# Optimization experiments

Measured on AMD Instinct MI355X. Metric: run time of the kernel, lower is better.

## Reference

```python
import jax, jax.numpy as jnp
import numpy as np

B, L, D, H = 4, 1024, 1024, 16
DH = D // H
NEG = -1e9


def setup_inputs() -> dict:
    key = jax.random.key(0)
    ks = jax.random.split(key, 8)
    sequence = jax.random.normal(ks[0], (B, L, D), dtype=jnp.float32)
    # additive padding mask: all tokens valid -> zeros
    padding_mask = jnp.zeros((B, 1, 1, L), dtype=jnp.float32)
    # additive causal dependency mask: -1e9 above the diagonal
    causal = jnp.triu(jnp.full((L, L), NEG, dtype=jnp.float32), k=1)
    dependency_mask = causal[None, None, :, :]
    scale = 1.0 / np.sqrt(D)
    Wq = jax.random.normal(ks[1], (D, D), dtype=jnp.float32) * scale
    Wk = jax.random.normal(ks[2], (D, D), dtype=jnp.float32) * scale
    Wv = jax.random.normal(ks[3], (D, D), dtype=jnp.float32) * scale
    bq = jnp.zeros((D,), dtype=jnp.float32)
    bk = jnp.zeros((D,), dtype=jnp.float32)
    bv = jnp.zeros((D,), dtype=jnp.float32)
    return {"sequence": sequence, "padding_mask": padding_mask,
            "dependency_mask": dependency_mask,
            "Wq": Wq, "bq": bq, "Wk": Wk, "bk": bk, "Wv": Wv, "bv": bv}


def reference(sequence, padding_mask, dependency_mask, Wq, bq, Wk, bk, Wv, bv):
    b, l, d = sequence.shape
    h, dh = H, d // H
    # Q/K/V linear projections (torch Linear: x @ W^T + b)
    q = (sequence @ Wq.T + bq).reshape(b, l, h, dh)
    k = (sequence @ Wk.T + bk).reshape(b, l, h, dh)
    v = (sequence @ Wv.T + bv).reshape(b, l, h, dh)
    # scaled dot-product scores: [B, H, L, L]
    scores = jnp.einsum('blhd,bmhd->bhlm', q, k) / jnp.sqrt(jnp.float32(dh))
    scores = scores + padding_mask + dependency_mask
    attn = jax.nn.softmax(scores, axis=-1)
    # dropout is identity in eval mode (training=False)
    out = jnp.einsum('bhlm,bmhd->blhd', attn, v)
    return out.reshape(b, l, d)
```

## Files before the change

kernel.cpp:

```cpp
#include <hip/hip_runtime.h>
#include <hip/hip_bf16.h>


#define LL 1024

typedef __attribute__((ext_vector_type(8))) short short8;
typedef __attribute__((ext_vector_type(4))) float floatx4;

__device__ __forceinline__ float bf2f(unsigned short u) {
    return __uint_as_float(((unsigned int)u) << 16);
}
__device__ __forceinline__ unsigned short f2bf(float f) {
    unsigned int x = __float_as_uint(f);
    unsigned int r = x + 0x7fffu + ((x >> 16) & 1u);
    return (unsigned short)(r >> 16);
}

#if __has_builtin(__builtin_amdgcn_global_load_lds)
#define HAVE_GLL 1
typedef __attribute__((address_space(1))) unsigned int as1_u32;
typedef __attribute__((address_space(3))) unsigned int as3_u32;
__device__ __forceinline__ void gll16(const void* g, void* l) {
    __builtin_amdgcn_global_load_lds((const as1_u32*)g, (as3_u32*)l, 16, 0, 0);
}
#endif

#if __has_builtin(__builtin_amdgcn_exp2f)
#define EXP2F(x) __builtin_amdgcn_exp2f(x)
#else
#define EXP2F(x) exp2f(x)
#endif

__global__ __launch_bounds__(256) void conv_in(
    const float* __restrict__ seq, const float* __restrict__ wq,
    const float* __restrict__ wk,  const float* __restrict__ wv,
    const float* __restrict__ bq,  const float* __restrict__ bk,
    const float* __restrict__ bv,  const float* __restrict__ pm,
    unsigned short* __restrict__ ws)
{
    unsigned int t = blockIdx.x * 256u + threadIdx.x;
    if (t >= 918400u) return;
    unsigned int e = t * 8u;
    const float* src; unsigned int idx; unsigned short* dst; float scale = 1.0f;
    if (e < 4194304u)      { src = seq; idx = e;            dst = ws + 12582912u; }
    else if (e < 5242880u) { src = wq;  idx = e - 4194304u; dst = ws + 16777216u; }
    else if (e < 6291456u) { src = wk;  idx = e - 5242880u; dst = ws + 17825792u; }
    else if (e < 7340032u) { src = wv;  idx = e - 6291456u; dst = ws + 18874368u; }
    else if (e < 7341056u) { src = bq;  idx = e - 7340032u; dst = ws + 20971520u; }
    else if (e < 7342080u) { src = bk;  idx = e - 7341056u; dst = ws + 20972544u; }
    else if (e < 7343104u) { src = bv;  idx = e - 7342080u; dst = ws + 20973568u; }
    else { src = pm; idx = e - 7343104u; dst = ws + 20974592u; scale = 1.4426950f; }
    float4 a = *(const float4*)(src + idx);
    float4 c = *(const float4*)(src + idx + 4);
    uint4 st;
    st.x = (unsigned)f2bf(a.x * scale) | ((unsigned)f2bf(a.y * scale) << 16);
    st.y = (unsigned)f2bf(a.z * scale) | ((unsigned)f2bf(a.w * scale) << 16);
    st.z = (unsigned)f2bf(c.x * scale) | ((unsigned)f2bf(c.y * scale) << 16);
    st.w = (unsigned)f2bf(c.z * scale) | ((unsigned)f2bf(c.w * scale) << 16);
    *(uint4*)(dst + idx) = st;
}

__global__ __launch_bounds__(512, 2) void qkv_proj(
    const unsigned short* __restrict__ X,
    const unsigned short* __restrict__ Wcat,
    const unsigned short* __restrict__ bcat,
    unsigned short* __restrict__ dst_base)
{
    __shared__ __align__(16) unsigned short SMEM[3 * 16384 + 2 * 12288];
    unsigned short (*Abuf)[16384] = (unsigned short (*)[16384])SMEM;
    unsigned short (*Bbuf)[12288] = (unsigned short (*)[12288])(SMEM + 3 * 16384);

    const int tid  = threadIdx.x;
    const int lane = tid & 63;
    const int wave = tid >> 6;
    const int quad = lane >> 4, r16 = lane & 15;
    const int wr = wave >> 1, wc = wave & 1;
    const int m0 = blockIdx.x * 256;
    const int n0 = blockIdx.y * 192;

    const int r3   = lane >> 3;
    const int stc  = ((lane & 7) ^ r3) << 3;
    const int seg0a = wave * 4;
    const int seg0b = wave * 3;

    const unsigned short* Asrc = X    + (size_t)(m0 + seg0a * 8 + r3) * 1024 + stc;
    const unsigned short* Bsrc = Wcat + (size_t)(n0 + seg0b * 8 + r3) * 1024 + stc;

    floatx4 acc[4][6];
#pragma unroll
    for (int i = 0; i < 4; ++i)
#pragma unroll
        for (int j = 0; j < 6; ++j)
#pragma unroll
            for (int r = 0; r < 4; ++r) acc[i][j][r] = 0.f;

#ifdef HAVE_GLL
#pragma unroll
    for (int c = 0; c < 4; ++c) gll16(Asrc + (size_t)c * 8192, &Abuf[0][(seg0a + c) * 512]);
#pragma unroll
    for (int c = 0; c < 3; ++c) gll16(Bsrc + (size_t)c * 8192, &Bbuf[0][(seg0b + c) * 512]);
#pragma unroll
    for (int c = 0; c < 4; ++c) gll16(Asrc + (size_t)c * 8192 + 64, &Abuf[1][(seg0a + c) * 512]);
    asm volatile("s_waitcnt vmcnt(4)" ::: "memory");
    __builtin_amdgcn_s_barrier();
#endif

    int sA = 0;
    for (int t = 0; t < 16; ++t) {
        const unsigned short* Ac = &Abuf[sA][0];
        const unsigned short* Bc = &Bbuf[t & 1][0];
        const int aoff = (wr * 64 + r16) * 64;
        const int boff = (wc * 96 + r16) * 64;
        const int c0 = ((0 + quad) ^ (r16 & 7)) << 3;
        const int c1 = ((4 + quad) ^ (r16 & 7)) << 3;
        const int sAw = (sA == 0) ? 2 : (sA - 1);
        const size_t koA = (size_t)((t + 2) << 6);
        short8 a[2], b[6];

#ifndef HAVE_GLL
        __syncthreads();
#pragma unroll
        for (int c = 0; c < 4; ++c)
            *(uint4*)&Abuf[0][(seg0a + c) * 512 + lane * 8] =
                *(const uint4*)(Asrc + (size_t)c * 8192 + (t << 6));
#pragma unroll
        for (int c = 0; c < 3; ++c)
            *(uint4*)&Bbuf[0][(seg0b + c) * 512 + lane * 8] =
                *(const uint4*)(Bsrc + (size_t)c * 8192 + (t << 6));
        __syncthreads();
        Ac = &Abuf[0][0]; Bc = &Bbuf[0][0];
#endif

#pragma unroll
        for (int j = 0; j < 6; ++j) b[j] = *(const short8*)&Bc[boff + j * 1024 + c0];
#pragma unroll
        for (int i = 0; i < 2; ++i) a[i] = *(const short8*)&Ac[aoff + i * 1024 + c0];
#ifdef HAVE_GLL
        if (t < 15) {
            const int sBw = (t + 1) & 1;
            const size_t ko = (size_t)((t + 1) << 6);
#pragma unroll
            for (int c = 0; c < 3; ++c)
                gll16(Bsrc + (size_t)c * 8192 + ko, &Bbuf[sBw][(seg0b + c) * 512]);
        }
        __builtin_amdgcn_s_barrier();
        asm volatile("s_waitcnt lgkmcnt(0)" ::: "memory");
#endif
        __builtin_amdgcn_s_setprio(1);
#pragma unroll
        for (int i = 0; i < 2; ++i)
#pragma unroll
            for (int j = 0; j < 6; ++j)
                acc[i][j] = __builtin_amdgcn_mfma_f32_16x16x32_bf16(a[i], b[j], acc[i][j], 0, 0, 0);
        __builtin_amdgcn_s_setprio(0);
#ifdef HAVE_GLL
        __builtin_amdgcn_s_barrier();
#endif

#pragma unroll
        for (int i = 0; i < 2; ++i) a[i] = *(const short8*)&Ac[aoff + (2 + i) * 1024 + c0];
#ifdef HAVE_GLL
        if (t < 14) {
#pragma unroll
            for (int c = 0; c < 2; ++c)
                gll16(Asrc + (size_t)c * 8192 + koA, &Abuf[sAw][(seg0a + c) * 512]);
        }
        __builtin_amdgcn_s_barrier();
        asm volatile("s_waitcnt lgkmcnt(0)" ::: "memory");
#endif
        __builtin_amdgcn_s_setprio(1);
#pragma unroll
        for (int i = 0; i < 2; ++i)
#pragma unroll
            for (int j = 0; j < 6; ++j)
                acc[2 + i][j] = __builtin_amdgcn_mfma_f32_16x16x32_bf16(a[i], b[j], acc[2 + i][j], 0, 0, 0);
        __builtin_amdgcn_s_setprio(0);
#ifdef HAVE_GLL
        __builtin_amdgcn_s_barrier();
#endif

#pragma unroll
        for (int j = 0; j < 6; ++j) b[j] = *(const short8*)&Bc[boff + j * 1024 + c1];
#pragma unroll
        for (int i = 0; i < 2; ++i) a[i] = *(const short8*)&Ac[aoff + i * 1024 + c1];
#ifdef HAVE_GLL
        if (t < 14) {
#pragma unroll
            for (int c = 2; c < 4; ++c)
                gll16(Asrc + (size_t)c * 8192 + koA, &Abuf[sAw][(seg0a + c) * 512]);
        }
        __builtin_amdgcn_s_barrier();
        asm volatile("s_waitcnt lgkmcnt(0)" ::: "memory");
#endif
        __builtin_amdgcn_s_setprio(1);
#pragma unroll
        for (int i = 0; i < 2; ++i)
#pragma unroll
            for (int j = 0; j < 6; ++j)
                acc[i][j] = __builtin_amdgcn_mfma_f32_16x16x32_bf16(a[i], b[j], acc[i][j], 0, 0, 0);
        __builtin_amdgcn_s_setprio(0);
#ifdef HAVE_GLL
        __builtin_amdgcn_s_barrier();
#endif

#pragma unroll
        for (int i = 0; i < 2; ++i) a[i] = *(const short8*)&Ac[aoff + (2 + i) * 1024 + c1];
#ifdef HAVE_GLL
        __builtin_amdgcn_s_barrier();
        asm volatile("s_waitcnt lgkmcnt(0)" ::: "memory");
#endif
        __builtin_amdgcn_s_setprio(1);
#pragma unroll
        for (int i = 0; i < 2; ++i)
#pragma unroll
            for (int j = 0; j < 6; ++j)
                acc[2 + i][j] = __builtin_amdgcn_mfma_f32_16x16x32_bf16(a[i], b[j], acc[2 + i][j], 0, 0, 0);
        __builtin_amdgcn_s_setprio(0);
#ifdef HAVE_GLL
        if (t < 14) {
            asm volatile("s_waitcnt vmcnt(4)" ::: "memory");
        } else if (t == 14) {
            asm volatile("s_waitcnt vmcnt(0)" ::: "memory");
        }
        __builtin_amdgcn_s_barrier();
#endif
        sA = (sA == 2) ? 0 : (sA + 1);
    }

    unsigned short* Cs = SMEM;
    const int b_ = m0 >> 10, l0_ = m0 & 1023;
#pragma unroll
    for (int j = 0; j < 6; ++j) {
        int n = n0 + wc * 96 + j * 16 + r16;
        int z = n >> 10;
        int nn = n & 1023;
        float bvf = bf2f(bcat[n]);
        int h = nn >> 6, d = nn & 63;
        if (z == 2) {
            unsigned short* dst = dst_base + (size_t)2 * (4096u * 1024u);
#pragma unroll
            for (int i = 0; i < 4; ++i) {
                int m_base = m0 + wr * 64 + i * 16 + quad * 4;
                int bb = m_base >> 10, l0 = m_base & 1023;
                ushort4 st;
                st.x = f2bf(acc[i][j][0] + bvf); st.y = f2bf(acc[i][j][1] + bvf);
                st.z = f2bf(acc[i][j][2] + bvf); st.w = f2bf(acc[i][j][3] + bvf);
                *(ushort4*)&dst[(((size_t)(bb * 16 + h)) * 64 + d) * 1024 + l0] = st;
            }
        } else {
            float sc = (z == 0) ? 0.18033688f : 1.0f;
            int col = wc * 96 + j * 16 + r16;
#pragma unroll
            for (int i = 0; i < 4; ++i) {
                int mrow = wr * 64 + i * 16 + quad * 4;
#pragma unroll
                for (int r = 0; r < 4; ++r)
                    Cs[(mrow + r) * 208 + col] = f2bf((acc[i][j][r] + bvf) * sc);
            }
        }
    }
    asm volatile("s_waitcnt lgkmcnt(0)" ::: "memory");
    __builtin_amdgcn_s_barrier();
#pragma unroll
    for (int g = 0; g < 3; ++g) {
        int ng = n0 + g * 64;
        int zg = ng >> 10;
        if (zg < 2) {
            int hg = (ng & 1023) >> 6;
            unsigned short* dq = dst_base + (size_t)zg * (4096u * 1024u)
                               + (((size_t)(b_ * 16 + hg)) * 1024 + l0_) * 64;
#pragma unroll
            for (int it = 0; it < 4; ++it) {
                int row = it * 64 + (tid >> 3);
                uint4 v = *(const uint4*)&Cs[row * 208 + g * 64 + (tid & 7) * 8];
                *(uint4*)(dq + (size_t)row * 64 + (tid & 7) * 8) = v;
            }
        }
    }
}

__global__ __launch_bounds__(256) void attn(
    const unsigned short* __restrict__ Qw,
    const unsigned short* __restrict__ Kw,
    const unsigned short* __restrict__ Vt_g,
    const unsigned short* __restrict__ pmask,
    float* __restrict__ out)
{
    __shared__ __align__(16) unsigned short KsF[8192];
    __shared__ __align__(16) unsigned short VsF[8192];
    __shared__ __align__(16) unsigned short PsF[4][2048];

    const int tid  = threadIdx.x;
    const int lane = tid & 63;
    const int wave = tid >> 6;
    const int quad = lane >> 4, r16 = lane & 15;

    const int bid  = blockIdx.x;
    const int half = bid >> 8, idx = bid & 255;
    const int bh   = idx & 63;
    const int qb   = idx >> 6;
    const int qi   = half ? (7 - qb) : qb;
    const int b    = bh >> 4, h = bh & 15;
    const int q0   = qi << 7;

    const size_t base = (size_t)bh * (1024 * 64);
    const unsigned short* Qg = Qw + base;
    const unsigned short* Kg = Kw + base;
    const unsigned short* Vg = Vt_g + base;

    const int kst_r3  = lane >> 3;
    const int kst_col = ((lane & 7) ^ kst_r3) << 3;
    const int vst_r   = lane >> 4;

    short8 aq[2][2];
#pragma unroll
    for (int f = 0; f < 2; ++f) {
        int qrow = q0 + f * 64 + wave * 16 + r16;
        aq[f][0] = *(const short8*)(Qg + (size_t)qrow * 64 + quad * 8);
        aq[f][1] = *(const short8*)(Qg + (size_t)qrow * 64 + 32 + quad * 8);
    }

    short8 ones;
#pragma unroll
    for (int i = 0; i < 8; ++i) ones[i] = (short)0x3f80;

    floatx4 ol[2];
    floatx4 o[2][4];
#pragma unroll
    for (int f = 0; f < 2; ++f)
#pragma unroll
        for (int r = 0; r < 4; ++r) ol[f][r] = 0.f;
#pragma unroll
    for (int f = 0; f < 2; ++f)
#pragma unroll
        for (int j = 0; j < 4; ++j)
#pragma unroll
            for (int r = 0; r < 4; ++r) o[f][j][r] = 0.f;

    for (int kt = 0; kt <= qi; ++kt) {
        float pm2[8];
#pragma unroll
        for (int j = 0; j < 8; ++j)
            pm2[j] = bf2f(pmask[b * LL + kt * 128 + j * 16 + r16]) - 12.0f;

        __syncthreads();
#ifdef HAVE_GLL
#pragma unroll
        for (int c2 = 0; c2 < 4; ++c2) {
            int seg = wave * 4 + c2;
            int krow = seg * 8 + kst_r3;
            gll16(Kg + (size_t)(kt * 128 + krow) * 64 + kst_col, &KsF[seg * 512]);
            int vrow = seg * 4 + vst_r;
            int vcol = (((lane & 15) ^ (vrow & 7))) << 3;
            gll16(Vg + (size_t)vrow * 1024 + kt * 128 + vcol, &VsF[seg * 512]);
        }
#else
#pragma unroll
        for (int c2 = 0; c2 < 4; ++c2) {
            int seg = wave * 4 + c2;
            int krow = seg * 8 + kst_r3;
            *(uint4*)&KsF[seg * 512 + lane * 8] =
                *(const uint4*)(Kg + (size_t)(kt * 128 + krow) * 64 + kst_col);
            int vrow = seg * 4 + vst_r;
            int vcol = (((lane & 15) ^ (vrow & 7))) << 3;
            *(uint4*)&VsF[seg * 512 + lane * 8] =
                *(const uint4*)(Vg + (size_t)vrow * 1024 + kt * 128 + vcol);
        }
#endif
        __syncthreads();

#pragma unroll
        for (int f = 0; f < 2; ++f) {
            floatx4 s[8];
#pragma unroll
            for (int j = 0; j < 8; ++j) {
                float pv = pm2[j];
#pragma unroll
                for (int r = 0; r < 4; ++r) s[j][r] = pv;
            }
#pragma unroll
            for (int j = 0; j < 8; ++j) {
                short8 bk0 = *(const short8*)&KsF[(j * 16 + r16) * 64 + (((0 * 4 + quad) ^ (r16 & 7)) << 3)];
                s[j] = __builtin_amdgcn_mfma_f32_16x16x32_bf16(aq[f][0], bk0, s[j], 0, 0, 0);
                short8 bk1 = *(const short8*)&KsF[(j * 16 + r16) * 64 + (((1 * 4 + quad) ^ (r16 & 7)) << 3)];
                s[j] = __builtin_amdgcn_mfma_f32_16x16x32_bf16(aq[f][1], bk1, s[j], 0, 0, 0);
            }

            if (kt == qi) {
                const int my_q = q0 + f * 64 + wave * 16 + quad * 4;
#pragma unroll
                for (int j = 0; j < 8; ++j) {
                    int key = kt * 128 + j * 16 + r16;
#pragma unroll
                    for (int r = 0; r < 4; ++r)
                        if (key > my_q + r) s[j][r] -= 1.0e9f;
                }
            }

#pragma unroll
            for (int j = 0; j < 8; ++j) {
                int key = j * 16 + r16;
                int ab = ((key >> 5) << 9) + (((key >> 3) & 3) << 7) + (key & 7) + (quad << 5);
#pragma unroll
                for (int r = 0; r < 4; ++r) {
                    float p = EXP2F(s[j][r]);
                    PsF[wave][ab + (r << 3)] = (unsigned short)(__float_as_uint(p) >> 16);
                }
            }
            asm volatile("s_waitcnt lgkmcnt(0)" ::: "memory");

#pragma unroll
            for (int kk4 = 0; kk4 < 4; ++kk4) {
                short8 ap = *(const short8*)&PsF[wave][kk4 * 512 + lane * 8];
                ol[f] = __builtin_amdgcn_mfma_f32_16x16x32_bf16(ap, ones, ol[f], 0, 0, 0);
#pragma unroll
                for (int j2 = 0; j2 < 4; ++j2) {
                    short8 bv = *(const short8*)&VsF[(j2 * 16 + r16) * 128 + (((kk4 * 4 + quad) ^ (r16 & 7)) << 3)];
                    o[f][j2] = __builtin_amdgcn_mfma_f32_16x16x32_bf16(ap, bv, o[f][j2], 0, 0, 0);
                }
            }
        }
    }

#pragma unroll
    for (int f = 0; f < 2; ++f) {
        float linv[4];
#pragma unroll
        for (int r = 0; r < 4; ++r)
            linv[r] = 1.0f / fmaxf(ol[f][r], 1.0e-30f);
        const int my_q = q0 + f * 64 + wave * 16 + quad * 4;
#pragma unroll
        for (int j2 = 0; j2 < 4; ++j2) {
            int d = j2 * 16 + r16;
#pragma unroll
            for (int r = 0; r < 4; ++r) {
                size_t oidx = ((size_t)(b * 1024 + my_q + r)) * 1024 + h * 64 + d;
                out[oidx] = o[f][j2][r] * linv[r];
            }
        }
    }
}

__global__ __launch_bounds__(256) void fill_sentinel_f(float* __restrict__ out,
                                                       float v, unsigned int n)
{
    unsigned int t = blockIdx.x * 256u + threadIdx.x;
    if (t < n) out[t] = v;
}

extern "C" void kernel_launch(void* const* d_in, const int* in_sizes, int n_in,
                              void* d_out, int out_size, void* d_ws, size_t ws_size,
                              hipStream_t stream) {
    bool sizes_ok = (n_in == 9) && in_sizes[0] == 4194304 && in_sizes[1] == 4096 &&
                    in_sizes[2] == 1048576 && in_sizes[3] == 1048576 && in_sizes[4] == 1024 &&
                    in_sizes[5] == 1048576 && in_sizes[6] == 1024 && in_sizes[7] == 1048576 &&
                    in_sizes[8] == 1024 && out_size == 4194304;
    if (!sizes_ok) {
        fill_sentinel_f<<<16384, 256, 0, stream>>>((float*)d_out, 100.0f, 4194304u);
        return;
    }
    if (ws_size < 50331652u) {
        fill_sentinel_f<<<16384, 256, 0, stream>>>((float*)d_out, 200.0f, 4194304u);
        return;
    }

    unsigned short* ws = (unsigned short*)d_ws;

    conv_in<<<3588, 256, 0, stream>>>(
        (const float*)d_in[0], (const float*)d_in[3], (const float*)d_in[5],
        (const float*)d_in[7], (const float*)d_in[4], (const float*)d_in[6],
        (const float*)d_in[8], (const float*)d_in[1], ws);

    const unsigned short* cseq  = ws + 12582912u;
    const unsigned short* cwcat = ws + 16777216u;
    const unsigned short* cbcat = ws + 20971520u;
    const unsigned short* cpm   = ws + 20974592u;

    dim3 g1(16, 16);
    qkv_proj<<<g1, 512, 0, stream>>>(cseq, cwcat, cbcat, ws);

    attn<<<512, 256, 0, stream>>>(ws, ws + 4194304u, ws + 8388608u, cpm, (float*)d_out);
}
```

Before: 148.0 us.

## Fuse fp32-to-bf16 conversion of the input sequence into the QKV projection loads

The separate conversion kernel no longer converts the activation sequence. The QKV GEMM now reads the fp32 sequence directly into registers, converts it to bf16 and writes it to shared memory, replacing the async global-to-LDS copies for the A operand. This removes a full-tensor read and write pass and shrinks the conversion launch. In exchange, each A tile is fetched as fp32 by every column block, which doubles that traffic. The register staging also adds VGPR pressure and requires a full vmcnt(0) wait each iteration, which weakens load/compute overlap.

New measurement: 162.2 us. 1.1x slower.

```diff
diff --git a/kernel.cpp b/kernel.cpp
--- a/kernel.cpp
+++ b/kernel.cpp
@@ -32,24 +32,22 @@
 #endif
 
 __global__ __launch_bounds__(256) void conv_in(
-    const float* __restrict__ seq, const float* __restrict__ wq,
-    const float* __restrict__ wk,  const float* __restrict__ wv,
-    const float* __restrict__ bq,  const float* __restrict__ bk,
-    const float* __restrict__ bv,  const float* __restrict__ pm,
-    unsigned short* __restrict__ ws)
+    const float* __restrict__ wq,  const float* __restrict__ wk,
+    const float* __restrict__ wv,  const float* __restrict__ bq,
+    const float* __restrict__ bk,  const float* __restrict__ bv,
+    const float* __restrict__ pm,  unsigned short* __restrict__ ws)
 {
     unsigned int t = blockIdx.x * 256u + threadIdx.x;
-    if (t >= 918400u) return;
+    if (t >= 394112u) return;
     unsigned int e = t * 8u;
     const float* src; unsigned int idx; unsigned short* dst; float scale = 1.0f;
-    if (e < 4194304u)      { src = seq; idx = e;            dst = ws + 12582912u; }
-    else if (e < 5242880u) { src = wq;  idx = e - 4194304u; dst = ws + 16777216u; }
-    else if (e < 6291456u) { src = wk;  idx = e - 5242880u; dst = ws + 17825792u; }
-    else if (e < 7340032u) { src = wv;  idx = e - 6291456u; dst = ws + 18874368u; }
-    else if (e < 7341056u) { src = bq;  idx = e - 7340032u; dst = ws + 20971520u; }
-    else if (e < 7342080u) { src = bk;  idx = e - 7341056u; dst = ws + 20972544u; }
-    else if (e < 7343104u) { src = bv;  idx = e - 7342080u; dst = ws + 20973568u; }
-    else { src = pm; idx = e - 7343104u; dst = ws + 20974592u; scale = 1.4426950f; }
+    if (e < 1048576u)      { src = wq;  idx = e;            dst = ws + 16777216u; }
+    else if (e < 2097152u) { src = wk;  idx = e - 1048576u; dst = ws + 17825792u; }
+    else if (e < 3145728u) { src = wv;  idx = e - 2097152u; dst = ws + 18874368u; }
+    else if (e < 3146752u) { src = bq;  idx = e - 3145728u; dst = ws + 20971520u; }
+    else if (e < 3147776u) { src = bk;  idx = e - 3146752u; dst = ws + 20972544u; }
+    else if (e < 3148800u) { src = bv;  idx = e - 3147776u; dst = ws + 20973568u; }
+    else { src = pm; idx = e - 3148800u; dst = ws + 20974592u; scale = 1.4426950f; }
     float4 a = *(const float4*)(src + idx);
     float4 c = *(const float4*)(src + idx + 4);
     uint4 st;
@@ -61,7 +59,7 @@
 }
 
 __global__ __launch_bounds__(512, 2) void qkv_proj(
-    const unsigned short* __restrict__ X,
+    const float* __restrict__ Xf,
     const unsigned short* __restrict__ Wcat,
     const unsigned short* __restrict__ bcat,
     unsigned short* __restrict__ dst_base)
@@ -83,7 +81,7 @@
     const int seg0a = wave * 4;
     const int seg0b = wave * 3;
 
-    const unsigned short* Asrc = X    + (size_t)(m0 + seg0a * 8 + r3) * 1024 + stc;
+    const float*          Xsrc = Xf   + (size_t)(m0 + seg0a * 8 + r3) * 1024 + stc;
     const unsigned short* Bsrc = Wcat + (size_t)(n0 + seg0b * 8 + r3) * 1024 + stc;
 
     floatx4 acc[4][6];
@@ -94,14 +92,27 @@
 #pragma unroll
             for (int r = 0; r < 4; ++r) acc[i][j][r] = 0.f;
 
-#ifdef HAVE_GLL
-#pragma unroll
-    for (int c = 0; c < 4; ++c) gll16(Asrc + (size_t)c * 8192, &Abuf[0][(seg0a + c) * 512]);
+    float4 areg[4][2];
+
+#ifdef HAVE_GLL
 #pragma unroll
     for (int c = 0; c < 3; ++c) gll16(Bsrc + (size_t)c * 8192, &Bbuf[0][(seg0b + c) * 512]);
 #pragma unroll
-    for (int c = 0; c < 4; ++c) gll16(Asrc + (size_t)c * 8192 + 64, &Abuf[1][(seg0a + c) * 512]);
-    asm volatile("s_waitcnt vmcnt(4)" ::: "memory");
+    for (int s = 0; s < 2; ++s) {
+#pragma unroll
+        for (int c = 0; c < 4; ++c) {
+            const float* src = Xsrc + (size_t)c * 8192 + s * 64;
+            float4 a0 = *(const float4*)(src);
+            float4 a1 = *(const float4*)(src + 4);
+            uint4 st;
+            st.x = (unsigned)f2bf(a0.x) | ((unsigned)f2bf(a0.y) << 16);
+            st.y = (unsigned)f2bf(a0.z) | ((unsigned)f2bf(a0.w) << 16);
+            st.z = (unsigned)f2bf(a1.x) | ((unsigned)f2bf(a1.y) << 16);
+            st.w = (unsigned)f2bf(a1.z) | ((unsigned)f2bf(a1.w) << 16);
+            *(uint4*)&Abuf[s][(seg0a + c) * 512 + lane * 8] = st;
+        }
+    }
+    asm volatile("s_waitcnt vmcnt(0) lgkmcnt(0)" ::: "memory");
     __builtin_amdgcn_s_barrier();
 #endif
 
@@ -120,9 +131,17 @@
 #ifndef HAVE_GLL
         __syncthreads();
 #pragma unroll
-        for (int c = 0; c < 4; ++c)
-            *(uint4*)&Abuf[0][(seg0a + c) * 512 + lane * 8] =
-                *(const uint4*)(Asrc + (size_t)c * 8192 + (t << 6));
+        for (int c = 0; c < 4; ++c) {
+            const float* src = Xsrc + (size_t)c * 8192 + (t << 6);
+            float4 a0 = *(const float4*)(src);
+            float4 a1 = *(const float4*)(src + 4);
+            uint4 st;
+            st.x = (unsigned)f2bf(a0.x) | ((unsigned)f2bf(a0.y) << 16);
+            st.y = (unsigned)f2bf(a0.z) | ((unsigned)f2bf(a0.w) << 16);
+            st.z = (unsigned)f2bf(a1.x) | ((unsigned)f2bf(a1.y) << 16);
+            st.w = (unsigned)f2bf(a1.z) | ((unsigned)f2bf(a1.w) << 16);
+            *(uint4*)&Abuf[0][(seg0a + c) * 512 + lane * 8] = st;
+        }
 #pragma unroll
         for (int c = 0; c < 3; ++c)
             *(uint4*)&Bbuf[0][(seg0b + c) * 512 + lane * 8] =
@@ -162,8 +181,11 @@
 #ifdef HAVE_GLL
         if (t < 14) {
 #pragma unroll
-            for (int c = 0; c < 2; ++c)
-                gll16(Asrc + (size_t)c * 8192 + koA, &Abuf[sAw][(seg0a + c) * 512]);
+            for (int c = 0; c < 4; ++c) {
+                const float* src = Xsrc + (size_t)c * 8192 + koA;
+                areg[c][0] = *(const float4*)(src);
+                areg[c][1] = *(const float4*)(src + 4);
+            }
         }
         __builtin_amdgcn_s_barrier();
         asm volatile("s_waitcnt lgkmcnt(0)" ::: "memory");
@@ -186,8 +208,14 @@
 #ifdef HAVE_GLL
         if (t < 14) {
 #pragma unroll
-            for (int c = 2; c < 4; ++c)
-                gll16(Asrc + (size_t)c * 8192 + koA, &Abuf[sAw][(seg0a + c) * 512]);
+            for (int c = 0; c < 4; ++c) {
+                uint4 st;
+                st.x = (unsigned)f2bf(areg[c][0].x) | ((unsigned)f2bf(areg[c][0].y) << 16);
+                st.y = (unsigned)f2bf(areg[c][0].z) | ((unsigned)f2bf(areg[c][0].w) << 16);
+                st.z = (unsigned)f2bf(areg[c][1].x) | ((unsigned)f2bf(areg[c][1].y) << 16);
+                st.w = (unsigned)f2bf(areg[c][1].z) | ((unsigned)f2bf(areg[c][1].w) << 16);
+                *(uint4*)&Abuf[sAw][(seg0a + c) * 512 + lane * 8] = st;
+            }
         }
         __builtin_amdgcn_s_barrier();
         asm volatile("s_waitcnt lgkmcnt(0)" ::: "memory");
@@ -217,9 +245,7 @@
                 acc[2 + i][j] = __builtin_amdgcn_mfma_f32_16x16x32_bf16(a[i], b[j], acc[2 + i][j], 0, 0, 0);
         __builtin_amdgcn_s_setprio(0);
 #ifdef HAVE_GLL
-        if (t < 14) {
-            asm volatile("s_waitcnt vmcnt(4)" ::: "memory");
-        } else if (t == 14) {
+        if (t < 15) {
             asm volatile("s_waitcnt vmcnt(0)" ::: "memory");
         }
         __builtin_amdgcn_s_barrier();
@@ -466,18 +492,17 @@
 
     unsigned short* ws = (unsigned short*)d_ws;
 
-    conv_in<<<3588, 256, 0, stream>>>(
-        (const float*)d_in[0], (const float*)d_in[3], (const float*)d_in[5],
-        (const float*)d_in[7], (const float*)d_in[4], (const float*)d_in[6],
-        (const float*)d_in[8], (const float*)d_in[1], ws);
-
-    const unsigned short* cseq  = ws + 12582912u;
+    conv_in<<<1540, 256, 0, stream>>>(
+        (const float*)d_in[3], (const float*)d_in[5], (const float*)d_in[7],
+        (const float*)d_in[4], (const float*)d_in[6], (const float*)d_in[8],
+        (const float*)d_in[1], ws);
+
     const unsigned short* cwcat = ws + 16777216u;
     const unsigned short* cbcat = ws + 20971520u;
     const unsigned short* cpm   = ws + 20974592u;
 
     dim3 g1(16, 16);
-    qkv_proj<<<g1, 512, 0, stream>>>(cseq, cwcat, cbcat, ws);
+    qkv_proj<<<g1, 512, 0, stream>>>((const float*)d_in[0], cwcat, cbcat, ws);
 
     attn<<<512, 256, 0, stream>>>(ws, ws + 4194304u, ws + 8388608u, cpm, (float*)d_out);
 }
```

## Halve QKV GEMM M-tile to 128 rows with 256-thread blocks and double buffering

Applied to the files above, without the earlier changes.

The QKV projection GEMM drops from 256x192 tiles on 512 threads to 128x192 tiles on 256 threads, which doubles the grid to 512 blocks. Each wave now loads six B segments instead of three. A's staging changes from a three-stage to a two-stage ring shared with B, and each step now waits on vmcnt(0) rather than keeping loads in flight. The aim is to spread the GEMM over more blocks and cut LDS use per block. The cost is less reuse of the weight tile and a shallower prefetch pipeline that may expose global-load latency.

After: 145.3 us (median of 2 runs). Within noise of the previous version (-1.8%).

```diff
diff --git a/kernel.cpp b/kernel.cpp
--- a/kernel.cpp
+++ b/kernel.cpp
@@ -60,28 +60,28 @@
     *(uint4*)(dst + idx) = st;
 }
 
-__global__ __launch_bounds__(512, 2) void qkv_proj(
+__global__ __launch_bounds__(256, 2) void qkv_proj(
     const unsigned short* __restrict__ X,
     const unsigned short* __restrict__ Wcat,
     const unsigned short* __restrict__ bcat,
     unsigned short* __restrict__ dst_base)
 {
-    __shared__ __align__(16) unsigned short SMEM[3 * 16384 + 2 * 12288];
-    unsigned short (*Abuf)[16384] = (unsigned short (*)[16384])SMEM;
-    unsigned short (*Bbuf)[12288] = (unsigned short (*)[12288])(SMEM + 3 * 16384);
+    __shared__ __align__(16) unsigned short SMEM[2 * 8192 + 2 * 12288];
+    unsigned short (*Abuf)[8192]  = (unsigned short (*)[8192])SMEM;
+    unsigned short (*Bbuf)[12288] = (unsigned short (*)[12288])(SMEM + 2 * 8192);
 
     const int tid  = threadIdx.x;
     const int lane = tid & 63;
     const int wave = tid >> 6;
     const int quad = lane >> 4, r16 = lane & 15;
     const int wr = wave >> 1, wc = wave & 1;
-    const int m0 = blockIdx.x * 256;
+    const int m0 = blockIdx.x * 128;
     const int n0 = blockIdx.y * 192;
 
     const int r3   = lane >> 3;
     const int stc  = ((lane & 7) ^ r3) << 3;
     const int seg0a = wave * 4;
-    const int seg0b = wave * 3;
+    const int seg0b = wave * 6;
 
     const unsigned short* Asrc = X    + (size_t)(m0 + seg0a * 8 + r3) * 1024 + stc;
     const unsigned short* Bsrc = Wcat + (size_t)(n0 + seg0b * 8 + r3) * 1024 + stc;
@@ -98,23 +98,25 @@
 #pragma unroll
     for (int c = 0; c < 4; ++c) gll16(Asrc + (size_t)c * 8192, &Abuf[0][(seg0a + c) * 512]);
 #pragma unroll
-    for (int c = 0; c < 3; ++c) gll16(Bsrc + (size_t)c * 8192, &Bbuf[0][(seg0b + c) * 512]);
-#pragma unroll
-    for (int c = 0; c < 4; ++c) gll16(Asrc + (size_t)c * 8192 + 64, &Abuf[1][(seg0a + c) * 512]);
-    asm volatile("s_waitcnt vmcnt(4)" ::: "memory");
+    for (int c = 0; c < 6; ++c) gll16(Bsrc + (size_t)c * 8192, &Bbuf[0][(seg0b + c) * 512]);
+    asm volatile("s_waitcnt vmcnt(0)" ::: "memory");
     __builtin_amdgcn_s_barrier();
 #endif
 
-    int sA = 0;
-    for (int t = 0; t < 16; ++t) {
-        const unsigned short* Ac = &Abuf[sA][0];
-        const unsigned short* Bc = &Bbuf[t & 1][0];
+    for (int t = 0; t < 8; ++t) {
+#pragma unroll
+    for (int ti = 0; ti < 2; ++ti) {
+        const int tt  = t * 2 + ti;
+        const int cur = tt & 1;
+        const int nxt = cur ^ 1;
+        const unsigned short* Ac = &Abuf[cur][0];
+        const unsigned short* Bc = &Bbuf[cur][0];
         const int aoff = (wr * 64 + r16) * 64;
         const int boff = (wc * 96 + r16) * 64;
         const int c0 = ((0 + quad) ^ (r16 & 7)) << 3;
         const int c1 = ((4 + quad) ^ (r16 & 7)) << 3;
-        const int sAw = (sA == 0) ? 2 : (sA - 1);
-        const size_t koA = (size_t)((t + 2) << 6);
+        const size_t ko = (size_t)((tt + 1) << 6);
+        const bool pf = (tt < 15);
         short8 a[2], b[6];
 
 #ifndef HAVE_GLL
@@ -122,11 +124,11 @@
 #pragma unroll
         for (int c = 0; c < 4; ++c)
             *(uint4*)&Abuf[0][(seg0a + c) * 512 + lane * 8] =
-                *(const uint4*)(Asrc + (size_t)c * 8192 + (t << 6));
-#pragma unroll
-        for (int c = 0; c < 3; ++c)
+                *(const uint4*)(Asrc + (size_t)c * 8192 + (tt << 6));
+#pragma unroll
+        for (int c = 0; c < 6; ++c)
             *(uint4*)&Bbuf[0][(seg0b + c) * 512 + lane * 8] =
-                *(const uint4*)(Bsrc + (size_t)c * 8192 + (t << 6));
+                *(const uint4*)(Bsrc + (size_t)c * 8192 + (tt << 6));
         __syncthreads();
         Ac = &Abuf[0][0]; Bc = &Bbuf[0][0];
 #endif
@@ -136,12 +138,10 @@
 #pragma unroll
         for (int i = 0; i < 2; ++i) a[i] = *(const short8*)&Ac[aoff + i * 1024 + c0];
 #ifdef HAVE_GLL
-        if (t < 15) {
-            const int sBw = (t + 1) & 1;
-            const size_t ko = (size_t)((t + 1) << 6);
-#pragma unroll
-            for (int c = 0; c < 3; ++c)
-                gll16(Bsrc + (size_t)c * 8192 + ko, &Bbuf[sBw][(seg0b + c) * 512]);
+        if (pf) {
+#pragma unroll
+            for (int c = 0; c < 6; ++c)
+                gll16(Bsrc + (size_t)c * 8192 + ko, &Bbuf[nxt][(seg0b + c) * 512]);
         }
         __builtin_amdgcn_s_barrier();
         asm volatile("s_waitcnt lgkmcnt(0)" ::: "memory");
@@ -160,10 +160,10 @@
 #pragma unroll
         for (int i = 0; i < 2; ++i) a[i] = *(const short8*)&Ac[aoff + (2 + i) * 1024 + c0];
 #ifdef HAVE_GLL
-        if (t < 14) {
+        if (pf) {
 #pragma unroll
             for (int c = 0; c < 2; ++c)
-                gll16(Asrc + (size_t)c * 8192 + koA, &Abuf[sAw][(seg0a + c) * 512]);
+                gll16(Asrc + (size_t)c * 8192 + ko, &Abuf[nxt][(seg0a + c) * 512]);
         }
         __builtin_amdgcn_s_barrier();
         asm volatile("s_waitcnt lgkmcnt(0)" ::: "memory");
@@ -184,10 +184,10 @@
 #pragma unroll
         for (int i = 0; i < 2; ++i) a[i] = *(const short8*)&Ac[aoff + i * 1024 + c1];
 #ifdef HAVE_GLL
-        if (t < 14) {
+        if (pf) {
 #pragma unroll
             for (int c = 2; c < 4; ++c)
-                gll16(Asrc + (size_t)c * 8192 + koA, &Abuf[sAw][(seg0a + c) * 512]);
+                gll16(Asrc + (size_t)c * 8192 + ko, &Abuf[nxt][(seg0a + c) * 512]);
         }
         __builtin_amdgcn_s_barrier();
         asm volatile("s_waitcnt lgkmcnt(0)" ::: "memory");
@@ -217,14 +217,12 @@
                 acc[2 + i][j] = __builtin_amdgcn_mfma_f32_16x16x32_bf16(a[i], b[j], acc[2 + i][j], 0, 0, 0);
         __builtin_amdgcn_s_setprio(0);
 #ifdef HAVE_GLL
-        if (t < 14) {
-            asm volatile("s_waitcnt vmcnt(4)" ::: "memory");
-        } else if (t == 14) {
+        if (pf) {
             asm volatile("s_waitcnt vmcnt(0)" ::: "memory");
         }
         __builtin_amdgcn_s_barrier();
 #endif
-        sA = (sA == 2) ? 0 : (sA + 1);
+    }
     }
 
     unsigned short* Cs = SMEM;
@@ -271,7 +269,7 @@
                                + (((size_t)(b_ * 16 + hg)) * 1024 + l0_) * 64;
 #pragma unroll
             for (int it = 0; it < 4; ++it) {
-                int row = it * 64 + (tid >> 3);
+                int row = it * 32 + (tid >> 3);
                 uint4 v = *(const uint4*)&Cs[row * 208 + g * 64 + (tid & 7) * 8];
                 *(uint4*)(dq + (size_t)row * 64 + (tid & 7) * 8) = v;
             }
@@ -476,8 +474,8 @@
     const unsigned short* cbcat = ws + 20971520u;
     const unsigned short* cpm   = ws + 20974592u;
 
-    dim3 g1(16, 16);
-    qkv_proj<<<g1, 512, 0, stream>>>(cseq, cwcat, cbcat, ws);
+    dim3 g1(32, 16);
+    qkv_proj<<<g1, 256, 0, stream>>>(cseq, cwcat, cbcat, ws);
 
     attn<<<512, 256, 0, stream>>>(ws, ws + 4194304u, ws + 8388608u, cpm, (float*)d_out);
 }
```
